# Kernel optimization log

Hardware: AMD Instinct MI355X
Metric: run time of the kernel (lower is better)

The kernel has to match this reference:

```python
import jax, jax.numpy as jnp
import numpy as np

N_USERS = 100000
N_ITEMS = 200000
N = N_USERS + N_ITEMS
D = 64
NNZ = 1200000
N_HOPS = 3
EDGE_DROP = 0.5   # torch code keeps an edge when floor(rate + rand) == 1, scales by 1/(1-rate)
MESS_DROP = 0.1


def setup_inputs() -> dict:
    key = jax.random.key(0)
    ku, ki, kv, kr, kc = jax.random.split(key, 5)
    user_embed = jax.random.normal(ku, (N_USERS, D), dtype=jnp.float32)
    item_embed = jax.random.normal(ki, (N_ITEMS, D), dtype=jnp.float32)
    vals = jax.random.uniform(kv, (NNZ,), dtype=jnp.float32)
    rows = jax.random.randint(kr, (NNZ,), 0, N, dtype=jnp.int32)
    cols = jax.random.randint(kc, (NNZ,), 0, N, dtype=jnp.int32)
    return {"user_embed": user_embed, "item_embed": item_embed, "vals": vals,
            "rows": rows, "cols": cols}


def reference(user_embed, item_embed, vals, rows, cols):
    all_embed = jnp.concatenate([user_embed, item_embed], axis=0)  # [N, D]
    agg = all_embed
    embs = [all_embed]  # embedding0=True prepends hop-0 embedding
    base_key = jax.random.key(42)
    inv_edge_keep = 1.0 / (1.0 - EDGE_DROP)
    inv_mess_keep = 1.0 / (1.0 - MESS_DROP)
    for hop in range(N_HOPS):
        ke, km = jax.random.split(jax.random.fold_in(base_key, hop), 2)
        # edge dropout: keep edge iff floor(rate + U[0,1)) == 1, i.e. U >= 1 - rate
        u = jax.random.uniform(ke, (NNZ,), dtype=jnp.float32)
        edge_keep = jnp.floor(EDGE_DROP + u)  # 0.0 / 1.0
        v = vals * edge_keep * inv_edge_keep
        # SpMM: out[r] += v_e * agg[c_e]
        agg = jax.ops.segment_sum(v[:, None] * agg[cols], rows, num_segments=N)
        # message dropout (inverted dropout, p = MESS_DROP)
        mess_keep = jax.random.bernoulli(km, 1.0 - MESS_DROP, agg.shape)
        agg = jnp.where(mess_keep, agg * inv_mess_keep, 0.0)
        embs.append(agg)
    embs = jnp.stack(embs, axis=1)  # [N, n_hops+1, D]
    return embs[:N_USERS], embs[N_USERS:]
```

## Files before the change

### kernel.cpp

```cpp
#include <hip/hip_runtime.h>
#include <stdint.h>

#define NU 100000
#define NI 200000
#define NT 300000
#define D 64
#define NNZ 1200000
#define NHOPS 3
#define SL 4
#define ROWF (SL * D)
#define KS 8
#define OVF_CAP 16384

__host__ __device__ __forceinline__ uint32_t rotl32(uint32_t x, int r) {
    return (x << r) | (x >> (32 - r));
}

__host__ __device__ inline void tf2x32(uint32_t k0, uint32_t k1,
                                       uint32_t x0, uint32_t x1,
                                       uint32_t& o0, uint32_t& o1) {
    uint32_t ks0 = k0, ks1 = k1, ks2 = k0 ^ k1 ^ 0x1BD11BDAu;
    x0 += ks0; x1 += ks1;
#define RND(r) { x0 += x1; x1 = rotl32(x1, r); x1 ^= x0; }
    RND(13) RND(15) RND(26) RND(6)
    x0 += ks1; x1 += ks2 + 1u;
    RND(17) RND(29) RND(16) RND(24)
    x0 += ks2; x1 += ks0 + 2u;
    RND(13) RND(15) RND(26) RND(6)
    x0 += ks0; x1 += ks1 + 3u;
    RND(17) RND(29) RND(16) RND(24)
    x0 += ks1; x1 += ks2 + 4u;
    RND(13) RND(15) RND(26) RND(6)
    o0 = x0 + ks2; o1 = x1 + ks0 + 5u;
#undef RND
}

__device__ __forceinline__ uint32_t rbits(uint32_t k0, uint32_t k1, uint32_t j) {
    uint32_t o0, o1;
    tf2x32(k0, k1, 0u, j, o0, o1);
    return o0 ^ o1;
}

__device__ __forceinline__ float u01(uint32_t bits) {
    return __uint_as_float((bits >> 9) | 0x3f800000u) - 1.0f;
}


__global__ void zero_kernel(int* __restrict__ p, int n) {
    int i = blockIdx.x * blockDim.x + threadIdx.x;
    if (i < n) p[i] = 0;
}

__global__ void scat_kernel(const int* __restrict__ rows,
                            const int* __restrict__ cols,
                            const float* __restrict__ vals,
                            int* __restrict__ kcnt,
                            int2* __restrict__ kslot,
                            int4* __restrict__ ovf,
                            uint32_t ke0, uint32_t ke1) {
    int e = blockIdx.x * blockDim.x + threadIdx.x;
    if (e >= NNZ) return;
    float u = u01(rbits(ke0, ke1, (uint32_t)e));
    if (u < 0.5f) return;
    int r = rows[e];
    int c = cols[e];
    float v2 = vals[e] * 2.0f;
    int pos = atomicAdd(&kcnt[r], 1);
    if (pos < KS) {
        kslot[(size_t)r * KS + pos] = make_int2(c, __float_as_int(v2));
    } else {
        int oi = atomicAdd(&kcnt[NT], 1);
        if (oi < OVF_CAP) ovf[oi] = make_int4(r, c, __float_as_int(v2), 0);
    }
}

template <int H0>
__global__ void spmm8_kernel(const int* __restrict__ kcnt,
                             const int2* __restrict__ kslot,
                             const int4* __restrict__ ovf,
                             const float* __restrict__ ue,
                             const float* __restrict__ ie,
                             float* __restrict__ out, int hop,
                             uint32_t km0, uint32_t km1) {
    int w    = (blockIdx.x * blockDim.x + threadIdx.x) >> 6;
    int lane = threadIdx.x & 63;
    int r0   = w * 8;
    if (r0 >= NT) return;

    int mk = 0;
    if (lane < 8) mk = kcnt[r0 + lane];
    int2 kp = kslot[(size_t)r0 * KS + lane];

    float4 e04a, e04b;
    if (H0) {
        const float4* s4 = (r0 < NU) ? (const float4*)(ue + (size_t)r0 * D)
                                     : (const float4*)(ie + (size_t)(r0 - NU) * D);
        e04a = s4[lane];
        e04b = s4[lane + 64];
    }

    int   cl = kp.x;
    float vl = __int_as_float(kp.y);

    int m[8];
    #pragma unroll
    for (int r = 0; r < 8; ++r) m[r] = __shfl(mk, r, 64);
    int mxf = 0;
    #pragma unroll
    for (int r = 0; r < 8; ++r) mxf = max(mxf, m[r]);
    int mx = (mxf < KS) ? mxf : KS;

    float acc[8] = {0.f, 0.f, 0.f, 0.f, 0.f, 0.f, 0.f, 0.f};

    for (int j = 0; j < mx; ++j) {
        float vv[8]; int cc[8];
        #pragma unroll
        for (int r = 0; r < 8; ++r) {
            int slot = r * KS + j;
            float v = __shfl(vl, slot, 64);
            int   c = __shfl(cl, slot, 64);
            bool ok = (j < m[r]);
            vv[r] = ok ? v : 0.0f;
            cc[r] = ok ? c : 0;
        }
        float g[8];
        #pragma unroll
        for (int r = 0; r < 8; ++r) {
            if (H0) {
                const float* b = (cc[r] < NU) ? ue : ie;
                int c2 = (cc[r] < NU) ? cc[r] : cc[r] - NU;
                g[r] = b[(size_t)c2 * D + lane];
            } else {
                g[r] = out[(size_t)cc[r] * ROWF + (size_t)hop * D + lane];
            }
        }
        #pragma unroll
        for (int r = 0; r < 8; ++r) acc[r] += vv[r] * g[r];
    }

    if (mxf > KS) {
        int no = kcnt[NT];
        if (no > OVF_CAP) no = OVF_CAP;
        #pragma unroll
        for (int r = 0; r < 8; ++r) {
            if (m[r] > KS) {
                for (int i = 0; i < no; ++i) {
                    int4 ent = ovf[i];
                    if (ent.x == r0 + r) {
                        float src;
                        if (H0) {
                            const float* b = (ent.y < NU) ? ue : ie;
                            int c2 = (ent.y < NU) ? ent.y : ent.y - NU;
                            src = b[(size_t)c2 * D + lane];
                        } else {
                            src = out[(size_t)ent.y * ROWF + (size_t)hop * D + lane];
                        }
                        acc[r] += __int_as_float(ent.z) * src;
                    }
                }
            }
        }
    }

    if (H0) {
        int f0 = lane, f1 = lane + 64;
        ((float4*)out)[(size_t)(r0 + (f0 >> 4)) * 64 + (f0 & 15)] = e04a;
        ((float4*)out)[(size_t)(r0 + (f1 >> 4)) * 64 + (f1 & 15)] = e04b;
    }

    const float P_KEEP = (float)(1.0 - 0.1);
    const float INVM   = (float)(1.0 / (1.0 - 0.1));
    #pragma unroll
    for (int r = 0; r < 8; ++r) {
        float um = u01(rbits(km0, km1, (uint32_t)((r0 + r) * D + lane)));
        float a  = (um < P_KEEP) ? acc[r] * INVM : 0.0f;
        out[(size_t)(r0 + r) * ROWF + (size_t)(hop + 1) * D + lane] = a;
    }
}


__global__ void init_kernel(const float4* __restrict__ ue,
                            const float4* __restrict__ ie,
                            float4* __restrict__ out) {
    int gid = blockIdx.x * blockDim.x + threadIdx.x;
    if (gid >= NT * 16) return;
    int n = gid >> 4, q = gid & 15;
    float4 v = (n < NU) ? ue[n * 16 + q] : ie[(n - NU) * 16 + q];
    float4 z = make_float4(0.f, 0.f, 0.f, 0.f);
    float4* row = out + (size_t)n * 64;
    row[q]      = v;
    row[16 + q] = z;
    row[32 + q] = z;
    row[48 + q] = z;
}

__global__ void spmm_inline_kernel(const float* __restrict__ vals,
                                   const int* __restrict__ rows,
                                   const int* __restrict__ cols,
                                   float* __restrict__ out, int hop,
                                   uint32_t ke0, uint32_t ke1) {
    int wid  = (blockIdx.x * blockDim.x + threadIdx.x) >> 6;
    int lane = threadIdx.x & 63;
    if (wid >= NNZ) return;
    float u = u01(rbits(ke0, ke1, (uint32_t)wid));
    if (u < 0.5f) return;
    float ve = vals[wid] * 2.0f;
    int r = rows[wid], c = cols[wid];
    float x = out[c * ROWF + hop * D + lane];
    unsafeAtomicAdd(&out[r * ROWF + (hop + 1) * D + lane], ve * x);
}

__global__ void mess_drop_kernel(float* __restrict__ out, int hop,
                                 uint32_t km0, uint32_t km1) {
    int j = blockIdx.x * blockDim.x + threadIdx.x;
    if (j >= NT * D) return;
    float u = u01(rbits(km0, km1, (uint32_t)j));
    int n = j >> 6, d = j & 63;
    int idx = n * ROWF + (hop + 1) * D + d;
    const float P_KEEP = (float)(1.0 - 0.1);
    const float INVM   = (float)(1.0 / (1.0 - 0.1));
    float a = out[idx];
    out[idx] = (u < P_KEEP) ? a * INVM : 0.0f;
}


extern "C" void kernel_launch(void* const* d_in, const int* in_sizes, int n_in,
                              void* d_out, int out_size, void* d_ws, size_t ws_size,
                              hipStream_t stream) {
    const float* ue   = (const float*)d_in[0];
    const float* ie   = (const float*)d_in[1];
    const float* vals = (const float*)d_in[2];
    const int*   rows = (const int*)d_in[3];
    const int*   cols = (const int*)d_in[4];
    float* out = (float*)d_out;

    const size_t off_kcnt  = 0;
    const size_t off_kslot = 1200016;
    const size_t off_ovf   = off_kslot + (size_t)NT * KS * 8;
    const size_t need      = off_ovf + (size_t)OVF_CAP * 16;

    uint32_t kf0, kf1;
    uint32_t ke0[NHOPS], ke1[NHOPS], km0[NHOPS], km1[NHOPS];
    for (int h = 0; h < NHOPS; ++h) {
        tf2x32(0u, 42u, 0u, (uint32_t)h, kf0, kf1);
        tf2x32(kf0, kf1, 0u, 0u, ke0[h], ke1[h]);
        tf2x32(kf0, kf1, 0u, 1u, km0[h], km1[h]);
    }

    if (ws_size >= need) {
        int*  kcnt  = (int*)((char*)d_ws + off_kcnt);
        int2* kslot = (int2*)((char*)d_ws + off_kslot);
        int4* ovf   = (int4*)((char*)d_ws + off_ovf);

        for (int h = 0; h < NHOPS; ++h) {
            zero_kernel<<<(NT + 1 + 255) / 256, 256, 0, stream>>>(kcnt, NT + 1);
            scat_kernel<<<(NNZ + 255) / 256, 256, 0, stream>>>(
                rows, cols, vals, kcnt, kslot, ovf, ke0[h], ke1[h]);
            if (h == 0)
                spmm8_kernel<1><<<(NT / 8 * 64 + 255) / 256, 256, 0, stream>>>(
                    kcnt, kslot, ovf, ue, ie, out, h, km0[h], km1[h]);
            else
                spmm8_kernel<0><<<(NT / 8 * 64 + 255) / 256, 256, 0, stream>>>(
                    kcnt, kslot, ovf, ue, ie, out, h, km0[h], km1[h]);
        }
    } else {
        init_kernel<<<(NT * 16 + 255) / 256, 256, 0, stream>>>(
            (const float4*)ue, (const float4*)ie, (float4*)out);
        for (int h = 0; h < NHOPS; ++h) {
            spmm_inline_kernel<<<(NNZ + 3) / 4, 256, 0, stream>>>(
                vals, rows, cols, out, h, ke0[h], ke1[h]);
            mess_drop_kernel<<<(NT * D + 255) / 256, 256, 0, stream>>>(out, h, km0[h], km1[h]);
        }
    }
}
```

Before: 343.9 us.

## Build adjacency once and apply edge dropout inside the SpMM kernel

Replaces the per-hop zero+scatter passes with a single adjacency build (16 slots per row holding col, edge id and value), and evaluates the edge-dropout random bits inside the SpMM kernel per slot. This removes two kernel launches and an atomic scatter per hop. In exchange each row carries more slot data, since all edges are kept rather than only the surviving ones, and each hop recomputes the RNG per slot. The dropout tests are also changed from float comparisons to integer bit tests. The new path needs a larger workspace, and its slot loop runs over both kept and dropped entries, so it iterates more times.

```diff
diff --git a/kernel.cpp b/kernel.cpp
--- a/kernel.cpp
+++ b/kernel.cpp
@@ -10,6 +10,7 @@
 #define SL 4
 #define ROWF (SL * D)
 #define KS 8
+#define KA 16
 #define OVF_CAP 16384
 
 __host__ __device__ __forceinline__ uint32_t rotl32(uint32_t x, int r) {
@@ -45,6 +46,142 @@
     return __uint_as_float((bits >> 9) | 0x3f800000u) - 1.0f;
 }
 
+#define MESS_KEEP_T 7549747u
+
+
+__global__ void build_adj_kernel(const int* __restrict__ rows,
+                                 const int* __restrict__ cols,
+                                 const float* __restrict__ vals,
+                                 int* __restrict__ acnt,
+                                 int4* __restrict__ aslot,
+                                 int4* __restrict__ ovf) {
+    int e = blockIdx.x * blockDim.x + threadIdx.x;
+    if (e >= NNZ) return;
+    int r = rows[e];
+    int pos = atomicAdd(&acnt[r], 1);
+    if (pos < KA) {
+        aslot[(size_t)r * KA + pos] = make_int4(cols[e], e, __float_as_int(vals[e]), 0);
+    } else {
+        int oi = atomicAdd(&acnt[NT], 1);
+        if (oi < OVF_CAP) ovf[oi] = make_int4(r, cols[e], e, __float_as_int(vals[e]));
+    }
+}
+
+template <int H0>
+__launch_bounds__(256)
+__global__ void spmmA_kernel(const int* __restrict__ acnt,
+                             const int4* __restrict__ aslot,
+                             const int4* __restrict__ ovf,
+                             const float* __restrict__ ue,
+                             const float* __restrict__ ie,
+                             float* __restrict__ out, int hop,
+                             uint32_t ke0, uint32_t ke1,
+                             uint32_t km0, uint32_t km1) {
+    int w    = (blockIdx.x * blockDim.x + threadIdx.x) >> 6;
+    int lane = threadIdx.x & 63;
+    int r0   = w * 8;
+    if (r0 >= NT) return;
+
+    int mk0 = 0;
+    if (lane < 8) mk0 = acnt[r0 + lane];
+    const int4* base = aslot + (size_t)r0 * KA;
+    int4 s0 = base[lane];
+    int4 s1 = base[lane + 64];
+
+    float4 e04a, e04b;
+    if (H0) {
+        const float4* s4 = (r0 < NU) ? (const float4*)(ue + (size_t)r0 * D)
+                                     : (const float4*)(ie + (size_t)(r0 - NU) * D);
+        e04a = s4[lane];
+        e04b = s4[lane + 64];
+    }
+
+    int a0 = __shfl(mk0, lane >> 4, 64);
+    int a1 = __shfl(mk0, (lane >> 4) + 4, 64);
+    uint32_t b0 = rbits(ke0, ke1, (uint32_t)s0.y);
+    uint32_t b1 = rbits(ke0, ke1, (uint32_t)s1.y);
+    bool k0 = ((b0 & 0x80000000u) != 0u) && ((lane & 15) < a0);
+    bool k1 = ((b1 & 0x80000000u) != 0u) && ((lane & 15) < a1);
+    float v0 = k0 ? __int_as_float(s0.z) * 2.0f : 0.0f;
+    float v1 = k1 ? __int_as_float(s1.z) * 2.0f : 0.0f;
+    int   c0 = k0 ? s0.x : 0;
+    int   c1 = k1 ? s1.x : 0;
+
+    int mkr = mk0;
+    mkr = max(mkr, __shfl_xor(mkr, 1, 64));
+    mkr = max(mkr, __shfl_xor(mkr, 2, 64));
+    mkr = max(mkr, __shfl_xor(mkr, 4, 64));
+    int mxf = __shfl(mkr, 0, 64);
+    int mx  = (mxf < KA) ? mxf : KA;
+
+    float acc[8] = {0.f, 0.f, 0.f, 0.f, 0.f, 0.f, 0.f, 0.f};
+
+    for (int j = 0; j < mx; ++j) {
+        float vv[8]; int cc[8];
+        #pragma unroll
+        for (int r = 0; r < 8; ++r) {
+            int sl = (r * KA + j) & 63;
+            vv[r] = __shfl((r < 4) ? v0 : v1, sl, 64);
+            cc[r] = __shfl((r < 4) ? c0 : c1, sl, 64);
+        }
+        float g[8];
+        #pragma unroll
+        for (int r = 0; r < 8; ++r) {
+            if (H0) {
+                const float* b = (cc[r] < NU) ? ue : ie;
+                int c2 = (cc[r] < NU) ? cc[r] : cc[r] - NU;
+                g[r] = b[(size_t)c2 * D + lane];
+            } else {
+                g[r] = out[(size_t)cc[r] * ROWF + (size_t)hop * D + lane];
+            }
+        }
+        #pragma unroll
+        for (int r = 0; r < 8; ++r) acc[r] += vv[r] * g[r];
+    }
+
+    if (mxf > KA) {
+        int no = acnt[NT];
+        if (no > OVF_CAP) no = OVF_CAP;
+        #pragma unroll
+        for (int r = 0; r < 8; ++r) {
+            int mr = __shfl(mk0, r, 64);
+            if (mr > KA) {
+                for (int i = 0; i < no; ++i) {
+                    int4 ent = ovf[i];
+                    if (ent.x == r0 + r) {
+                        uint32_t be = rbits(ke0, ke1, (uint32_t)ent.z);
+                        if (be & 0x80000000u) {
+                            float src;
+                            if (H0) {
+                                const float* b = (ent.y < NU) ? ue : ie;
+                                int c2 = (ent.y < NU) ? ent.y : ent.y - NU;
+                                src = b[(size_t)c2 * D + lane];
+                            } else {
+                                src = out[(size_t)ent.y * ROWF + (size_t)hop * D + lane];
+                            }
+                            acc[r] += __int_as_float(ent.w) * 2.0f * src;
+                        }
+                    }
+                }
+            }
+        }
+    }
+
+    if (H0) {
+        int f0 = lane, f1 = lane + 64;
+        ((float4*)out)[(size_t)(r0 + (f0 >> 4)) * 64 + (f0 & 15)] = e04a;
+        ((float4*)out)[(size_t)(r0 + (f1 >> 4)) * 64 + (f1 & 15)] = e04b;
+    }
+
+    const float INVM = (float)(1.0 / (1.0 - 0.1));
+    #pragma unroll
+    for (int r = 0; r < 8; ++r) {
+        uint32_t t = rbits(km0, km1, (uint32_t)((r0 + r) * D + lane)) >> 9;
+        float a = (t < MESS_KEEP_T) ? acc[r] * INVM : 0.0f;
+        out[(size_t)(r0 + r) * ROWF + (size_t)(hop + 1) * D + lane] = a;
+    }
+}
+
 
 __global__ void zero_kernel(int* __restrict__ p, int n) {
     int i = blockIdx.x * blockDim.x + threadIdx.x;
@@ -60,8 +197,8 @@
                             uint32_t ke0, uint32_t ke1) {
     int e = blockIdx.x * blockDim.x + threadIdx.x;
     if (e >= NNZ) return;
-    float u = u01(rbits(ke0, ke1, (uint32_t)e));
-    if (u < 0.5f) return;
+    uint32_t b = rbits(ke0, ke1, (uint32_t)e);
+    if (!(b & 0x80000000u)) return;
     int r = rows[e];
     int c = cols[e];
     float v2 = vals[e] * 2.0f;
@@ -168,12 +305,11 @@
         ((float4*)out)[(size_t)(r0 + (f1 >> 4)) * 64 + (f1 & 15)] = e04b;
     }
 
-    const float P_KEEP = (float)(1.0 - 0.1);
-    const float INVM   = (float)(1.0 / (1.0 - 0.1));
+    const float INVM = (float)(1.0 / (1.0 - 0.1));
     #pragma unroll
     for (int r = 0; r < 8; ++r) {
-        float um = u01(rbits(km0, km1, (uint32_t)((r0 + r) * D + lane)));
-        float a  = (um < P_KEEP) ? acc[r] * INVM : 0.0f;
+        uint32_t t = rbits(km0, km1, (uint32_t)((r0 + r) * D + lane)) >> 9;
+        float a = (t < MESS_KEEP_T) ? acc[r] * INVM : 0.0f;
         out[(size_t)(r0 + r) * ROWF + (size_t)(hop + 1) * D + lane] = a;
     }
 }
@@ -214,13 +350,12 @@
                                  uint32_t km0, uint32_t km1) {
     int j = blockIdx.x * blockDim.x + threadIdx.x;
     if (j >= NT * D) return;
-    float u = u01(rbits(km0, km1, (uint32_t)j));
+    uint32_t t = rbits(km0, km1, (uint32_t)j) >> 9;
     int n = j >> 6, d = j & 63;
     int idx = n * ROWF + (hop + 1) * D + d;
-    const float P_KEEP = (float)(1.0 - 0.1);
-    const float INVM   = (float)(1.0 / (1.0 - 0.1));
+    const float INVM = (float)(1.0 / (1.0 - 0.1));
     float a = out[idx];
-    out[idx] = (u < P_KEEP) ? a * INVM : 0.0f;
+    out[idx] = (t < MESS_KEEP_T) ? a * INVM : 0.0f;
 }
 
 
@@ -234,10 +369,15 @@
     const int*   cols = (const int*)d_in[4];
     float* out = (float*)d_out;
 
+    const size_t off_acnt  = 0;
+    const size_t off_aslot = 1200016;
+    const size_t off_aovf  = off_aslot + (size_t)NT * KA * 16;
+    const size_t need_adj  = off_aovf + (size_t)OVF_CAP * 16;
+
     const size_t off_kcnt  = 0;
     const size_t off_kslot = 1200016;
-    const size_t off_ovf   = off_kslot + (size_t)NT * KS * 8;
-    const size_t need      = off_ovf + (size_t)OVF_CAP * 16;
+    const size_t off_kovf  = off_kslot + (size_t)NT * KS * 8;
+    const size_t need_mid  = off_kovf + (size_t)OVF_CAP * 16;
 
     uint32_t kf0, kf1;
     uint32_t ke0[NHOPS], ke1[NHOPS], km0[NHOPS], km1[NHOPS];
@@ -247,21 +387,40 @@
         tf2x32(kf0, kf1, 0u, 1u, km0[h], km1[h]);
     }
 
-    if (ws_size >= need) {
+    if (ws_size >= need_adj) {
+        int*  acnt  = (int*)((char*)d_ws + off_acnt);
+        int4* aslot = (int4*)((char*)d_ws + off_aslot);
+        int4* aovf  = (int4*)((char*)d_ws + off_aovf);
+
+        hipMemsetAsync(acnt, 0, (NT + 1) * sizeof(int), stream);
+        build_adj_kernel<<<(NNZ + 255) / 256, 256, 0, stream>>>(
+            rows, cols, vals, acnt, aslot, aovf);
+
+        for (int h = 0; h < NHOPS; ++h) {
+            if (h == 0)
+                spmmA_kernel<1><<<(NT / 8 * 64 + 255) / 256, 256, 0, stream>>>(
+                    acnt, aslot, aovf, ue, ie, out, h,
+                    ke0[h], ke1[h], km0[h], km1[h]);
+            else
+                spmmA_kernel<0><<<(NT / 8 * 64 + 255) / 256, 256, 0, stream>>>(
+                    acnt, aslot, aovf, ue, ie, out, h,
+                    ke0[h], ke1[h], km0[h], km1[h]);
+        }
+    } else if (ws_size >= need_mid) {
         int*  kcnt  = (int*)((char*)d_ws + off_kcnt);
         int2* kslot = (int2*)((char*)d_ws + off_kslot);
-        int4* ovf   = (int4*)((char*)d_ws + off_ovf);
+        int4* kovf  = (int4*)((char*)d_ws + off_kovf);
 
         for (int h = 0; h < NHOPS; ++h) {
             zero_kernel<<<(NT + 1 + 255) / 256, 256, 0, stream>>>(kcnt, NT + 1);
             scat_kernel<<<(NNZ + 255) / 256, 256, 0, stream>>>(
-                rows, cols, vals, kcnt, kslot, ovf, ke0[h], ke1[h]);
+                rows, cols, vals, kcnt, kslot, kovf, ke0[h], ke1[h]);
             if (h == 0)
                 spmm8_kernel<1><<<(NT / 8 * 64 + 255) / 256, 256, 0, stream>>>(
-                    kcnt, kslot, ovf, ue, ie, out, h, km0[h], km1[h]);
+                    kcnt, kslot, kovf, ue, ie, out, h, km0[h], km1[h]);
             else
                 spmm8_kernel<0><<<(NT / 8 * 64 + 255) / 256, 256, 0, stream>>>(
-                    kcnt, kslot, ovf, ue, ie, out, h, km0[h], km1[h]);
+                    kcnt, kslot, kovf, ue, ie, out, h, km0[h], km1[h]);
         }
     } else {
         init_kernel<<<(NT * 16 + 255) / 256, 256, 0, stream>>>(
```

Result: no change. 346.9 us (+0.9%).

## Build all three hops' dropped-edge slot lists in one scatter pass

Applied to the files above, without the earlier changes.

Replaces the per-hop zero and scatter launches with a single memset and one scatter kernel. That kernel reads rows, cols and vals once and fills separate slot tables for all three hops. The SpMM gathers two edges per row per iteration for more memory parallelism, and hoists the message-dropout RNG ahead of the gather loop. Dropout comparisons use integer thresholds on the random bits instead of float conversion. It needs three times the workspace for slot tables, adds register pressure from the wider unroll, and relies on the integer thresholds matching the float comparisons exactly.

```diff
diff --git a/kernel.cpp b/kernel.cpp
--- a/kernel.cpp
+++ b/kernel.cpp
@@ -45,10 +45,43 @@
     return __uint_as_float((bits >> 9) | 0x3f800000u) - 1.0f;
 }
 
-
-__global__ void zero_kernel(int* __restrict__ p, int n) {
-    int i = blockIdx.x * blockDim.x + threadIdx.x;
-    if (i < n) p[i] = 0;
+#define MESS_KEEP_T 7549747u
+
+
+__global__ void scat3_kernel(const int* __restrict__ rows,
+                             const int* __restrict__ cols,
+                             const float* __restrict__ vals,
+                             int* __restrict__ kcnt3,
+                             int2* __restrict__ kslot3,
+                             int4* __restrict__ ovf3,
+                             uint32_t ka0, uint32_t ka1,
+                             uint32_t kb0, uint32_t kb1,
+                             uint32_t kc0, uint32_t kc1) {
+    int e = blockIdx.x * blockDim.x + threadIdx.x;
+    if (e >= NNZ) return;
+    int r = rows[e];
+    int c = cols[e];
+    float v2 = vals[e] * 2.0f;
+    int cv = __float_as_int(v2);
+    uint32_t b[3];
+    b[0] = rbits(ka0, ka1, (uint32_t)e);
+    b[1] = rbits(kb0, kb1, (uint32_t)e);
+    b[2] = rbits(kc0, kc1, (uint32_t)e);
+    #pragma unroll
+    for (int h = 0; h < 3; ++h) {
+        if (b[h] & 0x80000000u) {
+            int*  kc_ = kcnt3  + h * (NT + 1);
+            int2* ks_ = kslot3 + (size_t)h * NT * KS;
+            int4* ov_ = ovf3   + (size_t)h * OVF_CAP;
+            int pos = atomicAdd(&kc_[r], 1);
+            if (pos < KS) {
+                ks_[(size_t)r * KS + pos] = make_int2(c, cv);
+            } else {
+                int oi = atomicAdd(&kc_[NT], 1);
+                if (oi < OVF_CAP) ov_[oi] = make_int4(r, c, cv, 0);
+            }
+        }
+    }
 }
 
 __global__ void scat_kernel(const int* __restrict__ rows,
@@ -60,22 +93,21 @@
                             uint32_t ke0, uint32_t ke1) {
     int e = blockIdx.x * blockDim.x + threadIdx.x;
     if (e >= NNZ) return;
-    float u = u01(rbits(ke0, ke1, (uint32_t)e));
-    if (u < 0.5f) return;
+    uint32_t b = rbits(ke0, ke1, (uint32_t)e);
+    if (!(b & 0x80000000u)) return;
     int r = rows[e];
-    int c = cols[e];
-    float v2 = vals[e] * 2.0f;
     int pos = atomicAdd(&kcnt[r], 1);
     if (pos < KS) {
-        kslot[(size_t)r * KS + pos] = make_int2(c, __float_as_int(v2));
+        kslot[(size_t)r * KS + pos] = make_int2(cols[e], __float_as_int(vals[e] * 2.0f));
     } else {
         int oi = atomicAdd(&kcnt[NT], 1);
-        if (oi < OVF_CAP) ovf[oi] = make_int4(r, c, __float_as_int(v2), 0);
+        if (oi < OVF_CAP) ovf[oi] = make_int4(r, cols[e], __float_as_int(vals[e] * 2.0f), 0);
     }
 }
 
 template <int H0>
-__global__ void spmm8_kernel(const int* __restrict__ kcnt,
+__launch_bounds__(256)
+__global__ void spmmB_kernel(const int* __restrict__ kcnt,
                              const int2* __restrict__ kslot,
                              const int4* __restrict__ ovf,
                              const float* __restrict__ ue,
@@ -99,6 +131,11 @@
         e04b = s4[lane + 64];
     }
 
+    uint32_t mb[8];
+    #pragma unroll
+    for (int r = 0; r < 8; ++r)
+        mb[r] = rbits(km0, km1, (uint32_t)((r0 + r) * D + lane)) >> 9;
+
     int   cl = kp.x;
     float vl = __int_as_float(kp.y);
 
@@ -112,30 +149,34 @@
 
     float acc[8] = {0.f, 0.f, 0.f, 0.f, 0.f, 0.f, 0.f, 0.f};
 
-    for (int j = 0; j < mx; ++j) {
-        float vv[8]; int cc[8];
+    for (int jb = 0; jb < mx; jb += 2) {
+        float vv[16]; int cc[16];
         #pragma unroll
         for (int r = 0; r < 8; ++r) {
-            int slot = r * KS + j;
-            float v = __shfl(vl, slot, 64);
-            int   c = __shfl(cl, slot, 64);
-            bool ok = (j < m[r]);
-            vv[r] = ok ? v : 0.0f;
-            cc[r] = ok ? c : 0;
-        }
-        float g[8];
+            #pragma unroll
+            for (int k = 0; k < 2; ++k) {
+                int j = jb + k;
+                int slot = r * KS + j;
+                float v_ = __shfl(vl, slot, 64);
+                int   c_ = __shfl(cl, slot, 64);
+                bool ok = j < m[r];
+                vv[r * 2 + k] = ok ? v_ : 0.0f;
+                cc[r * 2 + k] = ok ? c_ : 0;
+            }
+        }
+        float g[16];
         #pragma unroll
-        for (int r = 0; r < 8; ++r) {
+        for (int t = 0; t < 16; ++t) {
             if (H0) {
-                const float* b = (cc[r] < NU) ? ue : ie;
-                int c2 = (cc[r] < NU) ? cc[r] : cc[r] - NU;
-                g[r] = b[(size_t)c2 * D + lane];
+                const float* b = (cc[t] < NU) ? ue : ie;
+                int c2 = (cc[t] < NU) ? cc[t] : cc[t] - NU;
+                g[t] = b[(size_t)c2 * D + lane];
             } else {
-                g[r] = out[(size_t)cc[r] * ROWF + (size_t)hop * D + lane];
+                g[t] = out[(size_t)cc[t] * ROWF + (size_t)hop * D + lane];
             }
         }
         #pragma unroll
-        for (int r = 0; r < 8; ++r) acc[r] += vv[r] * g[r];
+        for (int t = 0; t < 16; ++t) acc[t >> 1] += vv[t] * g[t];
     }
 
     if (mxf > KS) {
@@ -168,12 +209,10 @@
         ((float4*)out)[(size_t)(r0 + (f1 >> 4)) * 64 + (f1 & 15)] = e04b;
     }
 
-    const float P_KEEP = (float)(1.0 - 0.1);
-    const float INVM   = (float)(1.0 / (1.0 - 0.1));
+    const float INVM = (float)(1.0 / (1.0 - 0.1));
     #pragma unroll
     for (int r = 0; r < 8; ++r) {
-        float um = u01(rbits(km0, km1, (uint32_t)((r0 + r) * D + lane)));
-        float a  = (um < P_KEEP) ? acc[r] * INVM : 0.0f;
+        float a = (mb[r] < MESS_KEEP_T) ? acc[r] * INVM : 0.0f;
         out[(size_t)(r0 + r) * ROWF + (size_t)(hop + 1) * D + lane] = a;
     }
 }
@@ -214,13 +253,12 @@
                                  uint32_t km0, uint32_t km1) {
     int j = blockIdx.x * blockDim.x + threadIdx.x;
     if (j >= NT * D) return;
-    float u = u01(rbits(km0, km1, (uint32_t)j));
+    uint32_t t = rbits(km0, km1, (uint32_t)j) >> 9;
     int n = j >> 6, d = j & 63;
     int idx = n * ROWF + (hop + 1) * D + d;
-    const float P_KEEP = (float)(1.0 - 0.1);
-    const float INVM   = (float)(1.0 / (1.0 - 0.1));
+    const float INVM = (float)(1.0 / (1.0 - 0.1));
     float a = out[idx];
-    out[idx] = (u < P_KEEP) ? a * INVM : 0.0f;
+    out[idx] = (t < MESS_KEEP_T) ? a * INVM : 0.0f;
 }
 
 
@@ -234,10 +272,15 @@
     const int*   cols = (const int*)d_in[4];
     float* out = (float*)d_out;
 
+    const size_t off_kcnt3  = 0;
+    const size_t off_kslot3 = 3600016;
+    const size_t off_ovf3   = off_kslot3 + (size_t)3 * NT * KS * 8;
+    const size_t need_fast  = off_ovf3 + (size_t)3 * OVF_CAP * 16;
+
     const size_t off_kcnt  = 0;
     const size_t off_kslot = 1200016;
-    const size_t off_ovf   = off_kslot + (size_t)NT * KS * 8;
-    const size_t need      = off_ovf + (size_t)OVF_CAP * 16;
+    const size_t off_kovf  = off_kslot + (size_t)NT * KS * 8;
+    const size_t need_mid  = off_kovf + (size_t)OVF_CAP * 16;
 
     uint32_t kf0, kf1;
     uint32_t ke0[NHOPS], ke1[NHOPS], km0[NHOPS], km1[NHOPS];
@@ -247,21 +290,44 @@
         tf2x32(kf0, kf1, 0u, 1u, km0[h], km1[h]);
     }
 
-    if (ws_size >= need) {
+    const int spmm_grid = (NT / 8 * 64 + 255) / 256;
+
+    if (ws_size >= need_fast) {
+        int*  kcnt3  = (int*)((char*)d_ws + off_kcnt3);
+        int2* kslot3 = (int2*)((char*)d_ws + off_kslot3);
+        int4* ovf3   = (int4*)((char*)d_ws + off_ovf3);
+
+        hipMemsetAsync(kcnt3, 0, 3 * (NT + 1) * sizeof(int), stream);
+        scat3_kernel<<<(NNZ + 255) / 256, 256, 0, stream>>>(
+            rows, cols, vals, kcnt3, kslot3, ovf3,
+            ke0[0], ke1[0], ke0[1], ke1[1], ke0[2], ke1[2]);
+
+        for (int h = 0; h < NHOPS; ++h) {
+            const int*  kc = kcnt3 + h * (NT + 1);
+            const int2* ks = kslot3 + (size_t)h * NT * KS;
+            const int4* ov = ovf3 + (size_t)h * OVF_CAP;
+            if (h == 0)
+                spmmB_kernel<1><<<spmm_grid, 256, 0, stream>>>(
+                    kc, ks, ov, ue, ie, out, h, km0[h], km1[h]);
+            else
+                spmmB_kernel<0><<<spmm_grid, 256, 0, stream>>>(
+                    kc, ks, ov, ue, ie, out, h, km0[h], km1[h]);
+        }
+    } else if (ws_size >= need_mid) {
         int*  kcnt  = (int*)((char*)d_ws + off_kcnt);
         int2* kslot = (int2*)((char*)d_ws + off_kslot);
-        int4* ovf   = (int4*)((char*)d_ws + off_ovf);
+        int4* kovf  = (int4*)((char*)d_ws + off_kovf);
 
         for (int h = 0; h < NHOPS; ++h) {
-            zero_kernel<<<(NT + 1 + 255) / 256, 256, 0, stream>>>(kcnt, NT + 1);
+            hipMemsetAsync(kcnt, 0, (NT + 1) * sizeof(int), stream);
             scat_kernel<<<(NNZ + 255) / 256, 256, 0, stream>>>(
-                rows, cols, vals, kcnt, kslot, ovf, ke0[h], ke1[h]);
+                rows, cols, vals, kcnt, kslot, kovf, ke0[h], ke1[h]);
             if (h == 0)
-                spmm8_kernel<1><<<(NT / 8 * 64 + 255) / 256, 256, 0, stream>>>(
-                    kcnt, kslot, ovf, ue, ie, out, h, km0[h], km1[h]);
+                spmmB_kernel<1><<<spmm_grid, 256, 0, stream>>>(
+                    kcnt, kslot, kovf, ue, ie, out, h, km0[h], km1[h]);
             else
-                spmm8_kernel<0><<<(NT / 8 * 64 + 255) / 256, 256, 0, stream>>>(
-                    kcnt, kslot, ovf, ue, ie, out, h, km0[h], km1[h]);
+                spmmB_kernel<0><<<spmm_grid, 256, 0, stream>>>(
+                    kcnt, kslot, kovf, ue, ie, out, h, km0[h], km1[h]);
         }
     } else {
         init_kernel<<<(NT * 16 + 255) / 256, 256, 0, stream>>>(
```

New measurement: 405.6 us. +17.9%, slower.

## Bin rows by kept-edge count so each wave processes rows of equal degree

Applied to the files above, without the earlier changes.

Adds a place_kernel that buckets rows by their kept-edge count (0..8+) into an order array. The SpMM kernel then assigns each wave 8 rows drawn from the same bucket, so the inner loop bound mx matches every row in the wave. This targets lanes idling behind the longest row. The dropout tests also change: edge keep now checks the top random bit and message keep uses an integer threshold instead of a float comparison. The cost is one extra kernel per hop, an extra indirection, and writes to scattered rather than contiguous rows.

```diff
diff --git a/kernel.cpp b/kernel.cpp
--- a/kernel.cpp
+++ b/kernel.cpp
@@ -11,6 +11,7 @@
 #define ROWF (SL * D)
 #define KS 8
 #define OVF_CAP 16384
+#define NBIN 9
 
 __host__ __device__ __forceinline__ uint32_t rotl32(uint32_t x, int r) {
     return (x << r) | (x >> (32 - r));
@@ -45,6 +46,8 @@
     return __uint_as_float((bits >> 9) | 0x3f800000u) - 1.0f;
 }
 
+#define MESS_KEEP_T 7549747u
+
 
 __global__ void zero_kernel(int* __restrict__ p, int n) {
     int i = blockIdx.x * blockDim.x + threadIdx.x;
@@ -60,44 +63,81 @@
                             uint32_t ke0, uint32_t ke1) {
     int e = blockIdx.x * blockDim.x + threadIdx.x;
     if (e >= NNZ) return;
-    float u = u01(rbits(ke0, ke1, (uint32_t)e));
-    if (u < 0.5f) return;
+    uint32_t b = rbits(ke0, ke1, (uint32_t)e);
+    if (!(b & 0x80000000u)) return;
     int r = rows[e];
-    int c = cols[e];
-    float v2 = vals[e] * 2.0f;
     int pos = atomicAdd(&kcnt[r], 1);
     if (pos < KS) {
-        kslot[(size_t)r * KS + pos] = make_int2(c, __float_as_int(v2));
+        kslot[(size_t)r * KS + pos] = make_int2(cols[e], __float_as_int(vals[e] * 2.0f));
     } else {
         int oi = atomicAdd(&kcnt[NT], 1);
-        if (oi < OVF_CAP) ovf[oi] = make_int4(r, c, __float_as_int(v2), 0);
-    }
+        if (oi < OVF_CAP) ovf[oi] = make_int4(r, cols[e], __float_as_int(vals[e] * 2.0f), 0);
+    }
+}
+
+__global__ void place_kernel(const int* __restrict__ kcnt,
+                             int* __restrict__ bins,
+                             int* __restrict__ order) {
+    __shared__ int lh[NBIN];
+    __shared__ int lbase[NBIN];
+    int tid = threadIdx.x;
+    int r = blockIdx.x * blockDim.x + tid;
+    if (tid < NBIN) lh[tid] = 0;
+    __syncthreads();
+    int b = 0, lp = 0;
+    bool valid = (r < NT);
+    if (valid) {
+        int cnt = kcnt[r];
+        b = (cnt < 8) ? cnt : 8;
+        lp = atomicAdd(&lh[b], 1);
+    }
+    __syncthreads();
+    if (tid < NBIN) lbase[tid] = (lh[tid] > 0) ? atomicAdd(&bins[tid], lh[tid]) : 0;
+    __syncthreads();
+    if (valid) order[(size_t)b * NT + lbase[b] + lp] = r;
 }
 
 template <int H0>
-__global__ void spmm8_kernel(const int* __restrict__ kcnt,
+__global__ void spmm9_kernel(const int* __restrict__ kcnt,
                              const int2* __restrict__ kslot,
                              const int4* __restrict__ ovf,
+                             const int* __restrict__ order,
                              const float* __restrict__ ue,
                              const float* __restrict__ ie,
                              float* __restrict__ out, int hop,
                              uint32_t km0, uint32_t km1) {
     int w    = (blockIdx.x * blockDim.x + threadIdx.x) >> 6;
     int lane = threadIdx.x & 63;
-    int r0   = w * 8;
-    if (r0 >= NT) return;
-
-    int mk = 0;
-    if (lane < 8) mk = kcnt[r0 + lane];
-    int2 kp = kslot[(size_t)r0 * KS + lane];
-
-    float4 e04a, e04b;
-    if (H0) {
-        const float4* s4 = (r0 < NU) ? (const float4*)(ue + (size_t)r0 * D)
-                                     : (const float4*)(ie + (size_t)(r0 - NU) * D);
-        e04a = s4[lane];
-        e04b = s4[lane + 64];
-    }
+    int g0   = w * 8;
+    if (g0 >= NT) return;
+
+    const int* bins = kcnt + NT + 1;
+    int cum1, cum2, cum3, cum4, cum5, cum6, cum7, cum8, cum9;
+    cum1 = bins[0];          cum2 = cum1 + bins[1];  cum3 = cum2 + bins[2];
+    cum4 = cum3 + bins[3];   cum5 = cum4 + bins[4];  cum6 = cum5 + bins[5];
+    cum7 = cum6 + bins[6];   cum8 = cum7 + bins[7];  cum9 = cum8 + bins[8];
+    (void)cum9;
+
+    int myrow = 0;
+    if (lane < 8) {
+        int g = g0 + lane;
+        int b = (g >= cum1) + (g >= cum2) + (g >= cum3) + (g >= cum4) +
+                (g >= cum5) + (g >= cum6) + (g >= cum7) + (g >= cum8);
+        int cb = 0;
+        cb = (b > 0) ? cum1 : cb;  cb = (b > 1) ? cum2 : cb;
+        cb = (b > 2) ? cum3 : cb;  cb = (b > 3) ? cum4 : cb;
+        cb = (b > 4) ? cum5 : cb;  cb = (b > 5) ? cum6 : cb;
+        cb = (b > 6) ? cum7 : cb;  cb = (b > 7) ? cum8 : cb;
+        myrow = order[(size_t)b * NT + (g - cb)];
+    }
+    int mk = (lane < 8) ? kcnt[myrow] : 0;
+
+    int row[8];
+    #pragma unroll
+    for (int r = 0; r < 8; ++r) row[r] = __shfl(myrow, r, 64);
+
+    int rr = row[lane >> 3];
+    int2 kp = kslot[(size_t)rr * KS + (lane & 7)];
 
     int   cl = kp.x;
     float vl = __int_as_float(kp.y);
@@ -146,7 +186,7 @@
             if (m[r] > KS) {
                 for (int i = 0; i < no; ++i) {
                     int4 ent = ovf[i];
-                    if (ent.x == r0 + r) {
+                    if (ent.x == row[r]) {
                         float src;
                         if (H0) {
                             const float* b = (ent.y < NU) ? ue : ie;
@@ -163,18 +203,20 @@
     }
 
     if (H0) {
-        int f0 = lane, f1 = lane + 64;
-        ((float4*)out)[(size_t)(r0 + (f0 >> 4)) * 64 + (f0 & 15)] = e04a;
-        ((float4*)out)[(size_t)(r0 + (f1 >> 4)) * 64 + (f1 & 15)] = e04b;
-    }
-
-    const float P_KEEP = (float)(1.0 - 0.1);
-    const float INVM   = (float)(1.0 / (1.0 - 0.1));
+        #pragma unroll
+        for (int r = 0; r < 8; ++r) {
+            float e0 = (row[r] < NU) ? ue[(size_t)row[r] * D + lane]
+                                     : ie[(size_t)(row[r] - NU) * D + lane];
+            out[(size_t)row[r] * ROWF + lane] = e0;
+        }
+    }
+
+    const float INVM = (float)(1.0 / (1.0 - 0.1));
     #pragma unroll
     for (int r = 0; r < 8; ++r) {
-        float um = u01(rbits(km0, km1, (uint32_t)((r0 + r) * D + lane)));
-        float a  = (um < P_KEEP) ? acc[r] * INVM : 0.0f;
-        out[(size_t)(r0 + r) * ROWF + (size_t)(hop + 1) * D + lane] = a;
+        uint32_t t = rbits(km0, km1, (uint32_t)(row[r] * D + lane)) >> 9;
+        float a = (t < MESS_KEEP_T) ? acc[r] * INVM : 0.0f;
+        out[(size_t)row[r] * ROWF + (size_t)(hop + 1) * D + lane] = a;
     }
 }
 
@@ -202,8 +244,8 @@
     int wid  = (blockIdx.x * blockDim.x + threadIdx.x) >> 6;
     int lane = threadIdx.x & 63;
     if (wid >= NNZ) return;
-    float u = u01(rbits(ke0, ke1, (uint32_t)wid));
-    if (u < 0.5f) return;
+    uint32_t b = rbits(ke0, ke1, (uint32_t)wid);
+    if (!(b & 0x80000000u)) return;
     float ve = vals[wid] * 2.0f;
     int r = rows[wid], c = cols[wid];
     float x = out[c * ROWF + hop * D + lane];
@@ -214,13 +256,12 @@
                                  uint32_t km0, uint32_t km1) {
     int j = blockIdx.x * blockDim.x + threadIdx.x;
     if (j >= NT * D) return;
-    float u = u01(rbits(km0, km1, (uint32_t)j));
+    uint32_t t = rbits(km0, km1, (uint32_t)j) >> 9;
     int n = j >> 6, d = j & 63;
     int idx = n * ROWF + (hop + 1) * D + d;
-    const float P_KEEP = (float)(1.0 - 0.1);
-    const float INVM   = (float)(1.0 / (1.0 - 0.1));
+    const float INVM = (float)(1.0 / (1.0 - 0.1));
     float a = out[idx];
-    out[idx] = (u < P_KEEP) ? a * INVM : 0.0f;
+    out[idx] = (t < MESS_KEEP_T) ? a * INVM : 0.0f;
 }
 
 
@@ -235,9 +276,10 @@
     float* out = (float*)d_out;
 
     const size_t off_kcnt  = 0;
-    const size_t off_kslot = 1200016;
-    const size_t off_ovf   = off_kslot + (size_t)NT * KS * 8;
-    const size_t need      = off_ovf + (size_t)OVF_CAP * 16;
+    const size_t off_kslot = ((size_t)(NT + 16) * 4 + 15) & ~(size_t)15;
+    const size_t off_kovf  = off_kslot + (size_t)NT * KS * 8;
+    const size_t off_order = off_kovf + (size_t)OVF_CAP * 16;
+    const size_t need      = off_order + (size_t)NBIN * NT * 4;
 
     uint32_t kf0, kf1;
     uint32_t ke0[NHOPS], ke1[NHOPS], km0[NHOPS], km1[NHOPS];
@@ -247,21 +289,26 @@
         tf2x32(kf0, kf1, 0u, 1u, km0[h], km1[h]);
     }
 
+    const int spmm_grid = (NT / 8 * 64 + 255) / 256;
+
     if (ws_size >= need) {
         int*  kcnt  = (int*)((char*)d_ws + off_kcnt);
         int2* kslot = (int2*)((char*)d_ws + off_kslot);
-        int4* ovf   = (int4*)((char*)d_ws + off_ovf);
+        int4* kovf  = (int4*)((char*)d_ws + off_kovf);
+        int*  order = (int*)((char*)d_ws + off_order);
 
         for (int h = 0; h < NHOPS; ++h) {
-            zero_kernel<<<(NT + 1 + 255) / 256, 256, 0, stream>>>(kcnt, NT + 1);
+            zero_kernel<<<(NT + 16 + 255) / 256, 256, 0, stream>>>(kcnt, NT + 16);
             scat_kernel<<<(NNZ + 255) / 256, 256, 0, stream>>>(
-                rows, cols, vals, kcnt, kslot, ovf, ke0[h], ke1[h]);
+                rows, cols, vals, kcnt, kslot, kovf, ke0[h], ke1[h]);
+            place_kernel<<<(NT + 255) / 256, 256, 0, stream>>>(
+                kcnt, kcnt + NT + 1, order);
             if (h == 0)
-                spmm8_kernel<1><<<(NT / 8 * 64 + 255) / 256, 256, 0, stream>>>(
-                    kcnt, kslot, ovf, ue, ie, out, h, km0[h], km1[h]);
+                spmm9_kernel<1><<<spmm_grid, 256, 0, stream>>>(
+                    kcnt, kslot, kovf, order, ue, ie, out, h, km0[h], km1[h]);
             else
-                spmm8_kernel<0><<<(NT / 8 * 64 + 255) / 256, 256, 0, stream>>>(
-                    kcnt, kslot, ovf, ue, ie, out, h, km0[h], km1[h]);
+                spmm9_kernel<0><<<spmm_grid, 256, 0, stream>>>(
+                    kcnt, kslot, kovf, order, ue, ie, out, h, km0[h], km1[h]);
         }
     } else {
         init_kernel<<<(NT * 16 + 255) / 256, 256, 0, stream>>>(
```

New measurement: 438.6 us. +27.5%, slower.
